# Performance work log

Measured on AMD Instinct MI355X. Metric: run time of the kernel, lower is better.

The kernel has to match this reference:

```python
import jax, jax.numpy as jnp
import numpy as np


def setup_inputs() -> dict:
    key = jax.random.key(0)
    ks = jax.random.split(key, 12)
    M, B, N, FD, BD, BVD, H = 4096, 8, 512, 128, 128, 6, 64
    return {
        "f_pre_in": jax.random.normal(ks[0], (M, FD), jnp.float32),
        "f_pre_batch": jnp.sort(jax.random.randint(ks[1], (M,), 0, B)),
        "b_pre_in": jax.random.normal(ks[2], (B, BD, N), jnp.float32),
        "bv_in": jax.random.normal(ks[3], (B, BVD, N), jnp.float32),
        "Wf": jax.random.normal(ks[4], (H, FD), jnp.float32) * 0.05,
        "bf": jax.random.normal(ks[5], (H,), jnp.float32) * 0.05,
        "Wb": jax.random.normal(ks[6], (H, BD), jnp.float32) * 0.05,
        "bb": jax.random.normal(ks[7], (H,), jnp.float32) * 0.05,
        "Wbv": jax.random.normal(ks[8], (H, BVD), jnp.float32) * 0.05,
        "bbv": jax.random.normal(ks[9], (H,), jnp.float32) * 0.05,
        "Wo": jax.random.normal(ks[10], (H, 2 * H), jnp.float32) * 0.05,
        "bo": jax.random.normal(ks[11], (H,), jnp.float32) * 0.05,
    }


def reference(f_pre_in, f_pre_batch, b_pre_in, bv_in, Wf, bf, Wb, bb, Wbv, bbv, Wo, bo):
    # 1x1 Conv1d == channel matmul.
    H = Wf.shape[0]
    h2 = H // 2
    scale = jnp.sqrt(jnp.asarray(H, jnp.float32))  # sqrt(hidden_size)
    f = Wf @ f_pre_in.T + bf[:, None]                                  # (H, M)
    b_feat = jnp.einsum('hd,bdn->bhn', Wb, b_pre_in) + bb[None, :, None]   # (B, H, N)
    bv_feat = jnp.einsum('hc,bcn->bhn', Wbv, bv_in) + bbv[None, :, None]   # (B, H, N)
    # Per-node gather of that node's graph boundary features (f_pre_batch is sorted,
    # so per-node order == torch's per-batch concat order).
    be = b_feat[f_pre_batch, :h2]    # (M, h2, N)
    bg = b_feat[f_pre_batch, h2:]    # (M, h2, N)
    bvg = bv_feat[f_pre_batch]       # (M, H, N)
    # Cross-attention: softmax over the N boundary positions (torch dim=0 of (N, n_b)).
    w_euc = jax.nn.softmax(jnp.einsum('mhn,hm->mn', be, f[:h2]) / scale, axis=-1)  # (M, N)
    w_geo = jax.nn.softmax(jnp.einsum('mhn,hm->mn', bg, f[h2:]) / scale, axis=-1)  # (M, N)
    out_euc = jnp.einsum('mhn,mn->mh', bvg, w_euc)   # (M, H)
    out_geo = jnp.einsum('mhn,mn->mh', bvg, w_geo)   # (M, H)
    cat = jnp.concatenate([out_euc, out_geo], axis=1)  # (M, 2H)
    return cat @ Wo.T + bo                              # (M, H)
```

## Files before the change

kernel.cpp:

```cpp
#include <hip/hip_runtime.h>

#define M_TOT 4096
#define B_TOT 8
#define N_TOT 512
#define FD    128
#define BD    128
#define BVD   6
#define H     64
#define MAX_TILES 264

typedef short short8 __attribute__((ext_vector_type(8)));
typedef float floatx4 __attribute__((ext_vector_type(4)));

__device__ __forceinline__ unsigned short f2bf(float x) {
    union { float f; unsigned int u; } v; v.f = x;
    return (unsigned short)((v.u + 0x7fffu + ((v.u >> 16) & 1u)) >> 16);
}
__device__ __forceinline__ float bf2f(unsigned short u) {
    union { unsigned int u32; float f; } v; v.u32 = ((unsigned int)u) << 16;
    return v.f;
}

__device__ __forceinline__ int lb_dev(const int* __restrict__ arr, int n, int v) {
    int lo = 0, hi = n;
    while (lo < hi) { int mid = (lo + hi) >> 1; if (arr[mid] < v) lo = mid + 1; else hi = mid; }
    return lo;
}

__global__ __launch_bounds__(256) void k_pre(const float* __restrict__ f_pre_in,
                                             const int*   __restrict__ batch,
                                             const float* __restrict__ b_pre_in,
                                             const float* __restrict__ bv_in,
                                             const float* __restrict__ Wf,
                                             const float* __restrict__ bf,
                                             const float* __restrict__ Wb,
                                             const float* __restrict__ bb,
                                             const float* __restrict__ Wbv,
                                             const float* __restrict__ bbv,
                                             const float* __restrict__ Wo,
                                             unsigned short* __restrict__ f_bf,
                                             unsigned short* __restrict__ bFT_bf,
                                             unsigned short* __restrict__ bv_bf,
                                             unsigned short* __restrict__ Wo_bf,
                                             int4*  __restrict__ table) {
    __shared__ __align__(16) char sm[43264];
    const int t = threadIdx.x;
    const int blk = blockIdx.x;

    if (blk < 256) {
        float* fpre = (float*)sm;
        float* WfT  = (float*)(sm + 8448);
        const int m0 = blk * 16;
        for (int i = t; i < 16 * FD; i += 256)
            fpre[(i >> 7) * 132 + (i & 127)] = f_pre_in[(size_t)m0 * FD + i];
        for (int i = t; i < H * FD; i += 256)
            WfT[(i & 127) * 68 + (i >> 7)] = Wf[i];
        __syncthreads();
        const int mi = t >> 4;
        const int h4 = (t & 15) * 4;
        float a0 = bf[h4], a1 = bf[h4 + 1], a2 = bf[h4 + 2], a3 = bf[h4 + 3];
#pragma unroll 4
        for (int d4 = 0; d4 < 32; ++d4) {
            const float4 fp = *(const float4*)&fpre[mi * 132 + d4 * 4];
            const float* fpp = &fp.x;
#pragma unroll
            for (int i = 0; i < 4; ++i) {
                const float4 wv = *(const float4*)&WfT[(d4 * 4 + i) * 68 + h4];
                const float f = fpp[i];
                a0 += f * wv.x; a1 += f * wv.y; a2 += f * wv.z; a3 += f * wv.w;
            }
        }
        ushort4 o; o.x = f2bf(a0); o.y = f2bf(a1); o.z = f2bf(a2); o.w = f2bf(a3);
        *(ushort4*)&f_bf[(size_t)(m0 + mi) * H + h4] = o;
    } else if (blk < 512) {
        float* Wb_l = (float*)sm;
        float* bp   = (float*)(sm + 33024);
        const int idx = blk - 256;
        const int b  = idx >> 5;
        const int n0 = (idx & 31) * 16;
        for (int i = t; i < H * BD; i += 256)
            Wb_l[(i >> 7) * 129 + (i & 127)] = Wb[i];
        for (int i = t; i < BD * 16; i += 256)
            bp[(i >> 4) * 17 + (i & 15)] =
                b_pre_in[(size_t)b * BD * N_TOT + (size_t)(i >> 4) * N_TOT + n0 + (i & 15)];
        __syncthreads();
        const int h  = t & 63;
        const int nl = t >> 6;
        const float bias = bb[h];
        float acc[4] = {bias, bias, bias, bias};
        const float* wr = &Wb_l[h * 129];
#pragma unroll 8
        for (int d = 0; d < BD; ++d) {
            const float w = wr[d];
            acc[0] += w * bp[d * 17 + nl];
            acc[1] += w * bp[d * 17 + nl + 4];
            acc[2] += w * bp[d * 17 + nl + 8];
            acc[3] += w * bp[d * 17 + nl + 12];
        }
#pragma unroll
        for (int j = 0; j < 4; ++j)
            bFT_bf[((size_t)b * N_TOT + n0 + nl + 4 * j) * H + h] = f2bf(acc[j]);
    } else if (blk < 768) {
        const int idx = blk - 512;
        const int b  = idx >> 5;
        const int h  = (idx & 31) * 2 + (t >> 7);
        const int n4 = (t & 127) * 4;
        float w[BVD];
#pragma unroll
        for (int c = 0; c < BVD; ++c) w[c] = Wbv[h * BVD + c];
        const float bias = bbv[h];
        float a0 = bias, a1 = bias, a2 = bias, a3 = bias;
        const float* src = bv_in + (size_t)b * BVD * N_TOT + n4;
#pragma unroll
        for (int c = 0; c < BVD; ++c) {
            const float4 v = *(const float4*)(src + c * N_TOT);
            a0 += w[c] * v.x; a1 += w[c] * v.y; a2 += w[c] * v.z; a3 += w[c] * v.w;
        }
        ushort4 o; o.x = f2bf(a0); o.y = f2bf(a1); o.z = f2bf(a2); o.w = f2bf(a3);
        *(ushort4*)&bv_bf[((size_t)b * H + h) * N_TOT + n4] = o;
    } else {
        int starts[9];
#pragma unroll
        for (int b = 0; b <= 8; ++b) starts[b] = lb_dev(batch, M_TOT, b);
        int pre[9]; pre[0] = 0;
#pragma unroll
        for (int b = 0; b < 8; ++b) pre[b + 1] = pre[b] + (starts[b + 1] - starts[b] + 15) / 16;
        const int total = pre[8];
        for (int idx = t; idx < MAX_TILES; idx += 256) {
            int4 e = make_int4(0, 0, 0, 0);
            if (idx < total) {
                int b = 0;
                while (pre[b + 1] <= idx) ++b;
                const int r0 = starts[b] + (idx - pre[b]) * 16;
                e.x = b; e.y = r0; e.z = min(16, starts[b + 1] - r0);
            }
            table[idx] = e;
        }
        for (int i = t; i < H * 2 * H; i += 256) Wo_bf[i] = f2bf(Wo[i]);
    }
}

__global__ __launch_bounds__(256) void k_main(const unsigned short* __restrict__ f_bf,
                                              const unsigned short* __restrict__ bFT_bf,
                                              const unsigned short* __restrict__ bv_bf,
                                              const unsigned short* __restrict__ Wo_bf,
                                              const float* __restrict__ bo,
                                              const int4*  __restrict__ table,
                                              float* __restrict__ out) {
    __shared__ __align__(16) char wreg[4][8704];
    __shared__ __align__(16) float rowsumP[4][2][16];
    __shared__ __align__(16) unsigned short cat_l[16 * 136];

    const int t = threadIdx.x;
    const int wave = t >> 6, l = t & 63, quad = l >> 4, s = l & 15;
    const int4 te = table[blockIdx.x];
    const int b = te.x, m0 = te.y, nr = te.z;
    if (nr == 0) return;

    unsigned short* Wl = (unsigned short*)&wreg[wave][0];
    const floatx4 zero = {0.f, 0.f, 0.f, 0.f};

    const int rclamp = (s < nr) ? s : (nr - 1);
    const unsigned short* fptr = f_bf + (size_t)(m0 + rclamp) * H + quad * 8;
    const short8 fE = *(const short8*)(fptr);
    const short8 fG = *(const short8*)(fptr + 32);

    const unsigned short* bA = bFT_bf + ((size_t)b * N_TOT + wave * 128 + s) * H + quad * 8;
    floatx4 dE[8], dG[8];
#pragma unroll
    for (int c = 0; c < 8; ++c) {
        const short8 aE = *(const short8*)(bA + (size_t)c * 16 * H);
        const short8 aG = *(const short8*)(bA + (size_t)c * 16 * H + 32);
        dE[c] = __builtin_amdgcn_mfma_f32_16x16x32_bf16(aE, fE, zero, 0, 0, 0);
        dG[c] = __builtin_amdgcn_mfma_f32_16x16x32_bf16(aG, fG, zero, 0, 0, 0);
    }

    float rsE = 0.f, rsG = 0.f;
#pragma unroll
    for (int c = 0; c < 8; ++c) {
        ushort4 pE, pG;
        unsigned short u;
        u = f2bf(__expf(dE[c][0] * 0.125f)); rsE += bf2f(u); pE.x = u;
        u = f2bf(__expf(dE[c][1] * 0.125f)); rsE += bf2f(u); pE.y = u;
        u = f2bf(__expf(dE[c][2] * 0.125f)); rsE += bf2f(u); pE.z = u;
        u = f2bf(__expf(dE[c][3] * 0.125f)); rsE += bf2f(u); pE.w = u;
        u = f2bf(__expf(dG[c][0] * 0.125f)); rsG += bf2f(u); pG.x = u;
        u = f2bf(__expf(dG[c][1] * 0.125f)); rsG += bf2f(u); pG.y = u;
        u = f2bf(__expf(dG[c][2] * 0.125f)); rsG += bf2f(u); pG.z = u;
        u = f2bf(__expf(dG[c][3] * 0.125f)); rsG += bf2f(u); pG.w = u;
        *(ushort4*)&Wl[s * 136 + c * 16 + quad * 4]        = pE;
        *(ushort4*)&Wl[2176 + s * 136 + c * 16 + quad * 4] = pG;
    }
    rsE += __shfl_xor(rsE, 16); rsE += __shfl_xor(rsE, 32);
    rsG += __shfl_xor(rsG, 16); rsG += __shfl_xor(rsG, 32);
    if (l < 16) { rowsumP[wave][0][s] = rsE; rowsumP[wave][1][s] = rsG; }

    floatx4 oE[4] = {zero, zero, zero, zero};
    floatx4 oG[4] = {zero, zero, zero, zero};
#pragma unroll
    for (int kc = 0; kc < 4; ++kc) {
        const short8 aE = *(const short8*)&Wl[s * 136 + kc * 32 + quad * 8];
        const short8 aG = *(const short8*)&Wl[2176 + s * 136 + kc * 32 + quad * 8];
#pragma unroll
        for (int hc = 0; hc < 4; ++hc) {
            const short8 bvf = *(const short8*)(bv_bf +
                ((size_t)b * H + hc * 16 + s) * N_TOT + wave * 128 + kc * 32 + quad * 8);
            oE[hc] = __builtin_amdgcn_mfma_f32_16x16x32_bf16(aE, bvf, oE[hc], 0, 0, 0);
            oG[hc] = __builtin_amdgcn_mfma_f32_16x16x32_bf16(aG, bvf, oG[hc], 0, 0, 0);
        }
    }
    {
        float* Op = (float*)&wreg[wave][0];
#pragma unroll
        for (int hc = 0; hc < 4; ++hc) {
            *(floatx4*)&Op[(hc * 16 + s) * 16 + quad * 4]        = oE[hc];
            *(floatx4*)&Op[1024 + (hc * 16 + s) * 16 + quad * 4] = oG[hc];
        }
    }
    __syncthreads();

    {
        const int h  = t >> 2;
        const int r4 = (t & 3) * 4;
        floatx4 sE = zero, sG = zero, rE = zero, rG = zero;
#pragma unroll
        for (int w = 0; w < 4; ++w) {
            const float* opw = (const float*)&wreg[w][0];
            sE += *(const floatx4*)&opw[h * 16 + r4];
            sG += *(const floatx4*)&opw[1024 + h * 16 + r4];
            rE += *(const floatx4*)&rowsumP[w][0][r4];
            rG += *(const floatx4*)&rowsumP[w][1][r4];
        }
#pragma unroll
        for (int i = 0; i < 4; ++i) {
            cat_l[(r4 + i) * 136 + h]      = f2bf(sE[i] / rE[i]);
            cat_l[(r4 + i) * 136 + 64 + h] = f2bf(sG[i] / rG[i]);
        }
    }
    __syncthreads();

    {
        floatx4 acc = zero;
#pragma unroll
        for (int kc = 0; kc < 4; ++kc) {
            const short8 aC = *(const short8*)&cat_l[s * 136 + kc * 32 + quad * 8];
            const short8 bW = *(const short8*)(Wo_bf + (size_t)(wave * 16 + s) * 128 + kc * 32 + quad * 8);
            acc = __builtin_amdgcn_mfma_f32_16x16x32_bf16(aC, bW, acc, 0, 0, 0);
        }
        const int j = wave * 16 + s;
        const float bj = bo[j];
#pragma unroll
        for (int reg = 0; reg < 4; ++reg) {
            const int r = quad * 4 + reg;
            if (r < nr) out[(size_t)(m0 + r) * H + j] = acc[reg] + bj;
        }
    }
}

extern "C" void kernel_launch(void* const* d_in, const int* in_sizes, int n_in,
                              void* d_out, int out_size, void* d_ws, size_t ws_size,
                              hipStream_t stream) {
    const float* f_pre_in = (const float*)d_in[0];
    const int*   f_batch  = (const int*)  d_in[1];
    const float* b_pre_in = (const float*)d_in[2];
    const float* bv_in    = (const float*)d_in[3];
    const float* Wf       = (const float*)d_in[4];
    const float* bf       = (const float*)d_in[5];
    const float* Wb       = (const float*)d_in[6];
    const float* bb       = (const float*)d_in[7];
    const float* Wbv      = (const float*)d_in[8];
    const float* bbv      = (const float*)d_in[9];
    const float* Wo       = (const float*)d_in[10];
    const float* bo       = (const float*)d_in[11];
    float* out = (float*)d_out;

    unsigned short* f_bf   = (unsigned short*)d_ws;
    unsigned short* bFT_bf = f_bf + (size_t)M_TOT * H;
    unsigned short* bv_bf  = bFT_bf + (size_t)B_TOT * N_TOT * H;
    unsigned short* Wo_bf  = bv_bf + (size_t)B_TOT * H * N_TOT;
    int4* table = (int4*)(Wo_bf + (size_t)H * 2 * H);

    k_pre <<<769, 256, 0, stream>>>(f_pre_in, f_batch, b_pre_in, bv_in,
                                    Wf, bf, Wb, bb, Wbv, bbv, Wo,
                                    f_bf, bFT_bf, bv_bf, Wo_bf, table);
    k_main<<<MAX_TILES, 256, 0, stream>>>(f_bf, bFT_bf, bv_bf, Wo_bf, bo, table, out);
}
```

Measured before the change: 109.3 us.

## Use 8 waves per tile and split PV matmul by head tile instead of N

Doubles the block to 512 threads so each wave computes scores over 64 boundary positions instead of 128. The P·V matmul is repartitioned so each wave owns one (euc/geo, 16-head) output tile and reduces over the full N through shared memory. This removes the cross-wave partial-sum buffer and one reduction pass. In exchange it adds a block-wide barrier before P·V, and only half the waves do the final output projection.

```diff
diff --git a/kernel.cpp b/kernel.cpp
--- a/kernel.cpp
+++ b/kernel.cpp
@@ -140,15 +140,15 @@
     }
 }
 
-__global__ __launch_bounds__(256) void k_main(const unsigned short* __restrict__ f_bf,
+__global__ __launch_bounds__(512) void k_main(const unsigned short* __restrict__ f_bf,
                                               const unsigned short* __restrict__ bFT_bf,
                                               const unsigned short* __restrict__ bv_bf,
                                               const unsigned short* __restrict__ Wo_bf,
                                               const float* __restrict__ bo,
                                               const int4*  __restrict__ table,
                                               float* __restrict__ out) {
-    __shared__ __align__(16) char wreg[4][8704];
-    __shared__ __align__(16) float rowsumP[4][2][16];
+    __shared__ __align__(16) unsigned short Wlds[8][2][16][72];
+    __shared__ __align__(16) float rowsumP[8][2][16];
     __shared__ __align__(16) unsigned short cat_l[16 * 136];
 
     const int t = threadIdx.x;
@@ -157,7 +157,6 @@
     const int b = te.x, m0 = te.y, nr = te.z;
     if (nr == 0) return;
 
-    unsigned short* Wl = (unsigned short*)&wreg[wave][0];
     const floatx4 zero = {0.f, 0.f, 0.f, 0.f};
 
     const int rclamp = (s < nr) ? s : (nr - 1);
@@ -165,10 +164,10 @@
     const short8 fE = *(const short8*)(fptr);
     const short8 fG = *(const short8*)(fptr + 32);
 
-    const unsigned short* bA = bFT_bf + ((size_t)b * N_TOT + wave * 128 + s) * H + quad * 8;
-    floatx4 dE[8], dG[8];
-#pragma unroll
-    for (int c = 0; c < 8; ++c) {
+    const unsigned short* bA = bFT_bf + ((size_t)b * N_TOT + wave * 64 + s) * H + quad * 8;
+    floatx4 dE[4], dG[4];
+#pragma unroll
+    for (int c = 0; c < 4; ++c) {
         const short8 aE = *(const short8*)(bA + (size_t)c * 16 * H);
         const short8 aG = *(const short8*)(bA + (size_t)c * 16 * H + 32);
         dE[c] = __builtin_amdgcn_mfma_f32_16x16x32_bf16(aE, fE, zero, 0, 0, 0);
@@ -177,7 +176,7 @@
 
     float rsE = 0.f, rsG = 0.f;
 #pragma unroll
-    for (int c = 0; c < 8; ++c) {
+    for (int c = 0; c < 4; ++c) {
         ushort4 pE, pG;
         unsigned short u;
         u = f2bf(__expf(dE[c][0] * 0.125f)); rsE += bf2f(u); pE.x = u;
@@ -188,58 +187,38 @@
         u = f2bf(__expf(dG[c][1] * 0.125f)); rsG += bf2f(u); pG.y = u;
         u = f2bf(__expf(dG[c][2] * 0.125f)); rsG += bf2f(u); pG.z = u;
         u = f2bf(__expf(dG[c][3] * 0.125f)); rsG += bf2f(u); pG.w = u;
-        *(ushort4*)&Wl[s * 136 + c * 16 + quad * 4]        = pE;
-        *(ushort4*)&Wl[2176 + s * 136 + c * 16 + quad * 4] = pG;
+        *(ushort4*)&Wlds[wave][0][s][c * 16 + quad * 4] = pE;
+        *(ushort4*)&Wlds[wave][1][s][c * 16 + quad * 4] = pG;
     }
     rsE += __shfl_xor(rsE, 16); rsE += __shfl_xor(rsE, 32);
     rsG += __shfl_xor(rsG, 16); rsG += __shfl_xor(rsG, 32);
     if (l < 16) { rowsumP[wave][0][s] = rsE; rowsumP[wave][1][s] = rsG; }
-
-    floatx4 oE[4] = {zero, zero, zero, zero};
-    floatx4 oG[4] = {zero, zero, zero, zero};
-#pragma unroll
-    for (int kc = 0; kc < 4; ++kc) {
-        const short8 aE = *(const short8*)&Wl[s * 136 + kc * 32 + quad * 8];
-        const short8 aG = *(const short8*)&Wl[2176 + s * 136 + kc * 32 + quad * 8];
-#pragma unroll
-        for (int hc = 0; hc < 4; ++hc) {
-            const short8 bvf = *(const short8*)(bv_bf +
-                ((size_t)b * H + hc * 16 + s) * N_TOT + wave * 128 + kc * 32 + quad * 8);
-            oE[hc] = __builtin_amdgcn_mfma_f32_16x16x32_bf16(aE, bvf, oE[hc], 0, 0, 0);
-            oG[hc] = __builtin_amdgcn_mfma_f32_16x16x32_bf16(aG, bvf, oG[hc], 0, 0, 0);
-        }
-    }
+    __syncthreads();
+
     {
-        float* Op = (float*)&wreg[wave][0];
-#pragma unroll
-        for (int hc = 0; hc < 4; ++hc) {
-            *(floatx4*)&Op[(hc * 16 + s) * 16 + quad * 4]        = oE[hc];
-            *(floatx4*)&Op[1024 + (hc * 16 + s) * 16 + quad * 4] = oG[hc];
-        }
+        const int eg = wave & 1;
+        const int ht = wave >> 1;
+        floatx4 acc = zero;
+#pragma unroll
+        for (int c = 0; c < 16; ++c) {
+            const int wv = c >> 1, noff = (c & 1) * 32;
+            const short8 aW = *(const short8*)&Wlds[wv][eg][s][noff + quad * 8];
+            const short8 bV = *(const short8*)(bv_bf +
+                ((size_t)b * H + ht * 16 + s) * N_TOT + c * 32 + quad * 8);
+            acc = __builtin_amdgcn_mfma_f32_16x16x32_bf16(aW, bV, acc, 0, 0, 0);
+        }
+        floatx4 rs4 = zero;
+#pragma unroll
+        for (int w = 0; w < 8; ++w)
+            rs4 += *(const floatx4*)&rowsumP[w][eg][quad * 4];
+        const int j = eg * 64 + ht * 16 + s;
+#pragma unroll
+        for (int reg = 0; reg < 4; ++reg)
+            cat_l[(quad * 4 + reg) * 136 + j] = f2bf(acc[reg] / rs4[reg]);
     }
     __syncthreads();
 
-    {
-        const int h  = t >> 2;
-        const int r4 = (t & 3) * 4;
-        floatx4 sE = zero, sG = zero, rE = zero, rG = zero;
-#pragma unroll
-        for (int w = 0; w < 4; ++w) {
-            const float* opw = (const float*)&wreg[w][0];
-            sE += *(const floatx4*)&opw[h * 16 + r4];
-            sG += *(const floatx4*)&opw[1024 + h * 16 + r4];
-            rE += *(const floatx4*)&rowsumP[w][0][r4];
-            rG += *(const floatx4*)&rowsumP[w][1][r4];
-        }
-#pragma unroll
-        for (int i = 0; i < 4; ++i) {
-            cat_l[(r4 + i) * 136 + h]      = f2bf(sE[i] / rE[i]);
-            cat_l[(r4 + i) * 136 + 64 + h] = f2bf(sG[i] / rG[i]);
-        }
-    }
-    __syncthreads();
-
-    {
+    if (wave < 4) {
         floatx4 acc = zero;
 #pragma unroll
         for (int kc = 0; kc < 4; ++kc) {
@@ -283,5 +262,5 @@
     k_pre <<<769, 256, 0, stream>>>(f_pre_in, f_batch, b_pre_in, bv_in,
                                     Wf, bf, Wb, bb, Wbv, bbv, Wo,
                                     f_bf, bFT_bf, bv_bf, Wo_bf, table);
-    k_main<<<MAX_TILES, 256, 0, stream>>>(f_bf, bFT_bf, bv_bf, Wo_bf, bo, table, out);
-}
+    k_main<<<MAX_TILES, 512, 0, stream>>>(f_bf, bFT_bf, bv_bf, Wo_bf, bo, table, out);
+}
```

Measured after the change: 112.2 us. 1.03x slower.
